# Kernel tuning notes

Hardware: AMD Instinct MI355X
Metric: run time of the kernel (lower is better)

## Reference

```python
import jax, jax.numpy as jnp
import numpy as np

N_NODES = 100000   # number of graph nodes
N_EDGES = 1600000  # adjacency nnz (avg degree 16)
FEAT_NNZ = 1600000 # sparse feature nnz (~16 per node)
F_IN = 512
F_OUT = 128


def setup_inputs() -> dict:
    key = jax.random.key(0)
    k1, k2, k3, k4, k5, k6 = jax.random.split(key, 6)
    adj_indices = jax.random.randint(k1, (2, N_EDGES), 0, N_NODES, dtype=jnp.int64 if jax.config.jax_enable_x64 else jnp.int32)
    adj_values = jax.random.uniform(k2, (N_EDGES,), dtype=jnp.float32)
    feat_rows = jax.random.randint(k3, (FEAT_NNZ,), 0, N_NODES)
    feat_cols = jax.random.randint(k4, (FEAT_NNZ,), 0, F_IN)
    feat_values = jax.random.uniform(k5, (FEAT_NNZ,), dtype=jnp.float32)
    # xavier_uniform init of the dense weight, as in the torch module
    bound = float(np.sqrt(6.0 / (F_IN + F_OUT)))
    weight = jax.random.uniform(k6, (F_IN, F_OUT), dtype=jnp.float32, minval=-bound, maxval=bound)
    return {
        "adj_indices": adj_indices,
        "adj_values": adj_values,
        "feat_rows": feat_rows,
        "feat_cols": feat_cols,
        "feat_values": feat_values,
        "weight": weight,
        "num_nodes": N_NODES,
    }


def _spmm(rows, cols, vals, num_rows, dense):
    """COO sparse [num_rows, ?] @ dense [?, K] -> [num_rows, K]."""
    msgs = vals[:, None] * dense[cols]          # [nnz, K] gather + scale
    return jax.ops.segment_sum(msgs, rows, num_segments=num_rows)


def reference(adj_indices, adj_values, feat_rows, feat_cols, feat_values, weight, num_nodes):
    # spmm(features, W): sparse [N, F_in] @ [F_in, F_out]
    base_features = _spmm(feat_rows, feat_cols, feat_values, num_nodes, weight)
    # spmm(A_hat, base): sparse [N, N] @ [N, F_out]  -- neighbor aggregation
    out = _spmm(adj_indices[0], adj_indices[1], adj_values, num_nodes, base_features)
    return out
```

## Files before the change

kernel.cpp:

```cpp
#include <hip/hip_runtime.h>
#include <stdint.h>

#define N_NODES 100000
#define F_IN    512
#define F_OUT   128
#define BROWS   128
#define NBKT    ((N_NODES + BROWS - 1) / BROWS)
#define CAP     2560
#define EPB     2048

typedef unsigned short     u16;
typedef unsigned int       u32;
typedef unsigned long long u64;
typedef long long          i64;

__device__ __forceinline__ float b2f(u16 u) {
    union { u32 i; float f; } x; x.i = ((u32)u) << 16; return x.f;
}
__device__ __forceinline__ u16 f2b(float f) {
    u32 i = __float_as_uint(f);
    return (u16)((i + 0x7fffu + ((i >> 16) & 1u)) >> 16);
}
__device__ __forceinline__ float blo(u32 u) { return __uint_as_float(u << 16); }
__device__ __forceinline__ float bhi(u32 u) { return __uint_as_float(u & 0xFFFF0000u); }
__device__ __forceinline__ int ld_idx(const void* p, int i, int w64) {
    return w64 ? (int)((const i64*)p)[i] : ((const int*)p)[i];
}
__device__ __forceinline__ u16 ld_val_bf(const void* p, int i, int f32) {
    return f32 ? f2b(((const float*)p)[i]) : ((const u16*)p)[i];
}
__device__ __forceinline__ void ld_idx4(int* r, const void* p, int g, int w64) {
    if (w64) {
        const i64* q = (const i64*)p + 4 * (size_t)g;
        longlong2 a = *(const longlong2*)q;
        longlong2 b = *(const longlong2*)(q + 2);
        r[0] = (int)a.x; r[1] = (int)a.y; r[2] = (int)b.x; r[3] = (int)b.y;
    } else {
        int4 a = *(const int4*)((const int*)p + 4 * (size_t)g);
        r[0] = a.x; r[1] = a.y; r[2] = a.z; r[3] = a.w;
    }
}
__device__ __forceinline__ void ld_val4(u32* v, const void* p, int g, int f32) {
    if (f32) {
        float4 a = *(const float4*)((const float*)p + 4 * (size_t)g);
        v[0] = f2b(a.x); v[1] = f2b(a.y); v[2] = f2b(a.z); v[3] = f2b(a.w);
    } else {
        ushort4 a = *(const ushort4*)((const u16*)p + 4 * (size_t)g);
        v[0] = a.x; v[1] = a.y; v[2] = a.z; v[3] = a.w;
    }
}

__global__ void sniff_k(const u16* __restrict__ w, const u32* __restrict__ adj,
                        const u32* __restrict__ frows, int* __restrict__ flags,
                        int* __restrict__ gcurF, int* __restrict__ gcurA) {
    int t = threadIdx.x;
    if (t < 64) {
        u32 e0 = (w[t]      >> 7) & 0xFF;
        u32 e1 = (w[64 + t] >> 7) & 0xFF;
        u64 bad = __ballot((e0 > 0x7B) || (e1 > 0x7B));
        u64 za = __ballot(adj[2 * t + 1] == 0u);
        u64 zf = __ballot(frows[2 * t + 1] == 0u);
        if (t == 0) {
            flags[0] = (bad != 0);
            flags[1] = (__popcll(za) >= 32);
            flags[2] = (__popcll(zf) >= 32);
        }
    }
    for (int i = t; i < NBKT; i += 256) { gcurF[i] = 0; gcurA[i] = 0; }
}

__global__ __launch_bounds__(512, 6) void binF_k(const void* __restrict__ frows,
        const void* __restrict__ fcols, const void* __restrict__ fvals, int M,
        const int* __restrict__ flags, int* __restrict__ gcurF, u32* __restrict__ fbkt) {
    __shared__ int hist[NBKT];
    __shared__ int hbase[NBKT];
    int t = threadIdx.x;
    for (int i = t; i < NBKT; i += 512) hist[i] = 0;
    __syncthreads();
    int f64 = flags[2], f32 = flags[0];
    int start = blockIdx.x * EPB;
    int end = min(start + EPB, M);
    int g = (start >> 2) + t;
    int e0 = 4 * g;
    int r[4] = {-1, -1, -1, -1};
    int c[4]; u32 v[4];
    if (e0 + 3 < end) {
        ld_idx4(r, frows, g, f64);
        ld_idx4(c, fcols, g, f64);
        ld_val4(v, fvals, g, f32);
    } else {
        #pragma unroll
        for (int j = 0; j < 4; ++j) if (e0 + j < end) {
            r[j] = ld_idx(frows, e0 + j, f64);
            c[j] = ld_idx(fcols, e0 + j, f64);
            v[j] = ld_val_bf(fvals, e0 + j, f32);
        }
    }
    #pragma unroll
    for (int j = 0; j < 4; ++j) if (r[j] >= 0) atomicAdd(&hist[r[j] >> 7], 1);
    __syncthreads();
    for (int i = t; i < NBKT; i += 512) {
        int h = hist[i];
        hbase[i] = h ? atomicAdd(&gcurF[i], h) : 0;
        hist[i] = 0;
    }
    __syncthreads();
    #pragma unroll
    for (int j = 0; j < 4; ++j) if (r[j] >= 0) {
        int b = r[j] >> 7;
        int pos = hbase[b] + atomicAdd(&hist[b], 1);
        if (pos < CAP)
            fbkt[(size_t)b * CAP + pos] = (v[j] << 16) | ((u32)(r[j] & 127) << 9) | (u32)c[j];
    }
}

union S1Mem {
    struct { int hist[NBKT]; int hbase[NBKT]; } bin;
    struct { u32 csr[CAP]; int hcnt[BROWS]; int roff[BROWS + 1]; int cur[BROWS]; } s1;
};

__global__ __launch_bounds__(512, 4) void binA_s1_k(
        const void* __restrict__ adjbase, const void* __restrict__ avals, int E, int nAb,
        const int* __restrict__ flags, int* __restrict__ gcurA, u64* __restrict__ abkt,
        const int* __restrict__ cntF, const u32* __restrict__ fbkt,
        const void* __restrict__ W, u16* __restrict__ base) {
    __shared__ S1Mem sm;
    int t = threadIdx.x;
    int f32 = flags[0];
    if ((int)blockIdx.x < nAb) {
        for (int i = t; i < NBKT; i += 512) sm.bin.hist[i] = 0;
        __syncthreads();
        int a64 = flags[1];
        const void* acols = a64 ? (const void*)((const i64*)adjbase + E)
                                : (const void*)((const int*)adjbase + E);
        int start = blockIdx.x * EPB;
        int end = min(start + EPB, E);
        int g = (start >> 2) + t;
        int e0 = 4 * g;
        int r[4] = {-1, -1, -1, -1};
        int c[4]; u32 v[4];
        if (e0 + 3 < end) {
            ld_idx4(r, adjbase, g, a64);
            ld_idx4(c, acols, g, a64);
            ld_val4(v, avals, g, f32);
        } else {
            #pragma unroll
            for (int j = 0; j < 4; ++j) if (e0 + j < end) {
                r[j] = ld_idx(adjbase, e0 + j, a64);
                c[j] = ld_idx(acols, e0 + j, a64);
                v[j] = ld_val_bf(avals, e0 + j, f32);
            }
        }
        #pragma unroll
        for (int j = 0; j < 4; ++j) if (r[j] >= 0) atomicAdd(&sm.bin.hist[r[j] >> 7], 1);
        __syncthreads();
        for (int i = t; i < NBKT; i += 512) {
            int h = sm.bin.hist[i];
            sm.bin.hbase[i] = h ? atomicAdd(&gcurA[i], h) : 0;
            sm.bin.hist[i] = 0;
        }
        __syncthreads();
        #pragma unroll
        for (int j = 0; j < 4; ++j) if (r[j] >= 0) {
            int b = r[j] >> 7;
            int pos = sm.bin.hbase[b] + atomicAdd(&sm.bin.hist[b], 1);
            if (pos < CAP)
                abkt[(size_t)b * CAP + pos] =
                    ((u64)v[j] << 24) | ((u64)(r[j] & 127) << 17) | (u64)(u32)c[j];
        }
        return;
    }
    int b = blockIdx.x - nAb;
    int n = cntF[b]; if (n > CAP) n = CAP;
    const u32* ed = fbkt + (size_t)b * CAP;
    if (t < BROWS) sm.s1.hcnt[t] = 0;
    __syncthreads();
    u32 pb[5];
    #pragma unroll
    for (int k = 0; k < 5; ++k) { int i = t + k * 512; pb[k] = (i < n) ? ed[i] : 0u; }
    #pragma unroll
    for (int k = 0; k < 5; ++k) { int i = t + k * 512; if (i < n) atomicAdd(&sm.s1.hcnt[(pb[k] >> 9) & 127], 1); }
    __syncthreads();
    if (t < 64) {
        int h0 = sm.s1.hcnt[2 * t], h1 = sm.s1.hcnt[2 * t + 1];
        int s = h0 + h1, v2 = s;
        #pragma unroll
        for (int off = 1; off < 64; off <<= 1) {
            int u = __shfl_up(v2, off);
            if (t >= off) v2 += u;
        }
        int excl = v2 - s;
        sm.s1.roff[2 * t] = excl;     sm.s1.roff[2 * t + 1] = excl + h0;
        sm.s1.cur[2 * t]  = excl;     sm.s1.cur[2 * t + 1]  = excl + h0;
        if (t == 63) sm.s1.roff[128] = v2;
    }
    __syncthreads();
    #pragma unroll
    for (int k = 0; k < 5; ++k) {
        int i = t + k * 512;
        if (i < n) {
            u32 p = pb[k];
            int pos = atomicAdd(&sm.s1.cur[(p >> 9) & 127], 1);
            sm.s1.csr[pos] = p;
        }
    }
    __syncthreads();
    int wave = t >> 6, lane = t & 63, g16 = lane >> 4, l16 = lane & 15;
    #pragma unroll
    for (int set = 0; set < 4; ++set) {
        int row = set * 32 + wave * 4 + g16;
        int s = sm.s1.roff[row], e = sm.s1.roff[row + 1];
        float a[8] = {0.f, 0.f, 0.f, 0.f, 0.f, 0.f, 0.f, 0.f};
        if (f32) {
            const float* Wf = (const float*)W;
            for (int j0 = s; j0 < e; j0 += 4) {
                u32 p[4]; float4 qa[4], qb[4];
                #pragma unroll
                for (int k = 0; k < 4; ++k) { int jk = j0 + k; p[k] = sm.s1.csr[jk < e ? jk : e - 1]; }
                #pragma unroll
                for (int k = 0; k < 4; ++k) {
                    const float* wp = Wf + (size_t)(p[k] & 0x1FF) * F_OUT + l16 * 8;
                    qa[k] = *(const float4*)wp;
                    qb[k] = *(const float4*)(wp + 4);
                }
                #pragma unroll
                for (int k = 0; k < 4; ++k) {
                    float v = (j0 + k < e) ? b2f((u16)(p[k] >> 16)) : 0.f;
                    a[0] += v * qa[k].x; a[1] += v * qa[k].y;
                    a[2] += v * qa[k].z; a[3] += v * qa[k].w;
                    a[4] += v * qb[k].x; a[5] += v * qb[k].y;
                    a[6] += v * qb[k].z; a[7] += v * qb[k].w;
                }
            }
        } else {
            const u16* Wb = (const u16*)W;
            for (int j0 = s; j0 < e; j0 += 8) {
                u32 p[8]; uint4 q[8];
                #pragma unroll
                for (int k = 0; k < 8; ++k) { int jk = j0 + k; p[k] = sm.s1.csr[jk < e ? jk : e - 1]; }
                #pragma unroll
                for (int k = 0; k < 8; ++k)
                    q[k] = *(const uint4*)(Wb + (size_t)(p[k] & 0x1FF) * F_OUT + l16 * 8);
                #pragma unroll
                for (int k = 0; k < 8; ++k) {
                    float v = (j0 + k < e) ? b2f((u16)(p[k] >> 16)) : 0.f;
                    a[0] += v * blo(q[k].x); a[1] += v * bhi(q[k].x);
                    a[2] += v * blo(q[k].y); a[3] += v * bhi(q[k].y);
                    a[4] += v * blo(q[k].z); a[5] += v * bhi(q[k].z);
                    a[6] += v * blo(q[k].w); a[7] += v * bhi(q[k].w);
                }
            }
        }
        int gr = b * BROWS + row;
        if (gr < N_NODES) {
            uint4 o;
            o.x = (u32)f2b(a[0]) | ((u32)f2b(a[1]) << 16);
            o.y = (u32)f2b(a[2]) | ((u32)f2b(a[3]) << 16);
            o.z = (u32)f2b(a[4]) | ((u32)f2b(a[5]) << 16);
            o.w = (u32)f2b(a[6]) | ((u32)f2b(a[7]) << 16);
            *(uint4*)(base + (size_t)gr * F_OUT + l16 * 8) = o;
        }
    }
}

__global__ __launch_bounds__(512, 4) void stage2_k(const int* __restrict__ cnt,
        const u64* __restrict__ bkts, const u16* __restrict__ base,
        const int* __restrict__ flags, void* __restrict__ out) {
    __shared__ u64 csr[CAP];
    __shared__ int hcnt[BROWS];
    __shared__ int roff[BROWS + 1];
    __shared__ int cur[BROWS];
    int t = threadIdx.x;
    int b = blockIdx.x;
    int n = cnt[b]; if (n > CAP) n = CAP;
    const u64* ed = bkts + (size_t)b * CAP;
    if (t < BROWS) hcnt[t] = 0;
    __syncthreads();
    u64 pb[5];
    #pragma unroll
    for (int k = 0; k < 5; ++k) { int i = t + k * 512; pb[k] = (i < n) ? ed[i] : 0ull; }
    #pragma unroll
    for (int k = 0; k < 5; ++k) { int i = t + k * 512; if (i < n) atomicAdd(&hcnt[(int)((pb[k] >> 17) & 127)], 1); }
    __syncthreads();
    if (t < 64) {
        int h0 = hcnt[2 * t], h1 = hcnt[2 * t + 1];
        int s = h0 + h1, v2 = s;
        #pragma unroll
        for (int off = 1; off < 64; off <<= 1) {
            int u = __shfl_up(v2, off);
            if (t >= off) v2 += u;
        }
        int excl = v2 - s;
        roff[2 * t] = excl;     roff[2 * t + 1] = excl + h0;
        cur[2 * t]  = excl;     cur[2 * t + 1]  = excl + h0;
        if (t == 63) roff[128] = v2;
    }
    __syncthreads();
    #pragma unroll
    for (int k = 0; k < 5; ++k) {
        int i = t + k * 512;
        if (i < n) {
            u64 p = pb[k];
            int pos = atomicAdd(&cur[(int)((p >> 17) & 127)], 1);
            csr[pos] = p;
        }
    }
    __syncthreads();
    int wave = t >> 6, lane = t & 63, g16 = lane >> 4, l16 = lane & 15;
    int f32o = flags[0];
    #pragma unroll
    for (int set = 0; set < 4; ++set) {
        int row = set * 32 + wave * 4 + g16;
        int s = roff[row], e = roff[row + 1];
        float a[8] = {0.f, 0.f, 0.f, 0.f, 0.f, 0.f, 0.f, 0.f};
        for (int j0 = s; j0 < e; j0 += 8) {
            u64 p[8]; uint4 q[8];
            #pragma unroll
            for (int k = 0; k < 8; ++k) { int jk = j0 + k; p[k] = csr[jk < e ? jk : e - 1]; }
            #pragma unroll
            for (int k = 0; k < 8; ++k)
                q[k] = *(const uint4*)(base + (size_t)(u32)(p[k] & 0x1FFFF) * F_OUT + l16 * 8);
            #pragma unroll
            for (int k = 0; k < 8; ++k) {
                float v = (j0 + k < e) ? b2f((u16)(p[k] >> 24)) : 0.f;
                a[0] += v * blo(q[k].x); a[1] += v * bhi(q[k].x);
                a[2] += v * blo(q[k].y); a[3] += v * bhi(q[k].y);
                a[4] += v * blo(q[k].z); a[5] += v * bhi(q[k].z);
                a[6] += v * blo(q[k].w); a[7] += v * bhi(q[k].w);
            }
        }
        int gr = b * BROWS + row;
        if (gr < N_NODES) {
            if (f32o) {
                float* op = (float*)out + (size_t)gr * F_OUT + l16 * 8;
                float4 o0, o1;
                o0.x = a[0]; o0.y = a[1]; o0.z = a[2]; o0.w = a[3];
                o1.x = a[4]; o1.y = a[5]; o1.z = a[6]; o1.w = a[7];
                *(float4*)op = o0;
                *(float4*)(op + 4) = o1;
            } else {
                uint4 o;
                o.x = (u32)f2b(a[0]) | ((u32)f2b(a[1]) << 16);
                o.y = (u32)f2b(a[2]) | ((u32)f2b(a[3]) << 16);
                o.z = (u32)f2b(a[4]) | ((u32)f2b(a[5]) << 16);
                o.w = (u32)f2b(a[6]) | ((u32)f2b(a[7]) << 16);
                *(uint4*)((u16*)out + (size_t)gr * F_OUT + l16 * 8) = o;
            }
        }
    }
}

extern "C" void kernel_launch(void* const* d_in, const int* in_sizes, int n_in,
                              void* d_out, int out_size, void* d_ws, size_t ws_size,
                              hipStream_t stream) {
    const void* adj_idx   = d_in[0];
    const void* adj_vals  = d_in[1];
    const void* feat_rows = d_in[2];
    const void* feat_cols = d_in[3];
    const void* feat_vals = d_in[4];
    const void* weight    = d_in[5];

    const int E = in_sizes[0] / 2;
    const int M = in_sizes[2];

    char* ws = (char*)d_ws;
    size_t o = 0;
    auto alloc = [&](size_t b) { size_t r = o; o += (b + 255) & ~(size_t)255; return r; };
    int* gcurF = (int*)(ws + alloc((size_t)NBKT * 4));
    int* gcurA = (int*)(ws + alloc((size_t)NBKT * 4));
    int* flags = (int*)(ws + alloc(4 * 4));
    u32* fbkt  = (u32*)(ws + alloc((size_t)NBKT * CAP * 4));
    u64* abkt  = (u64*)(ws + alloc((size_t)NBKT * CAP * 8));
    u16* base  = (u16*)(ws + alloc((size_t)N_NODES * F_OUT * 2));
    (void)ws_size;

    const int nFb = (M + EPB - 1) / EPB;
    const int nAb = (E + EPB - 1) / EPB;

    sniff_k<<<1, 256, 0, stream>>>((const u16*)weight, (const u32*)adj_idx,
                                   (const u32*)feat_rows, flags, gcurF, gcurA);
    binF_k<<<nFb, 512, 0, stream>>>(feat_rows, feat_cols, feat_vals, M,
                                    flags, gcurF, fbkt);
    binA_s1_k<<<nAb + NBKT, 512, 0, stream>>>(adj_idx, adj_vals, E, nAb,
                                              flags, gcurA, abkt,
                                              gcurF, fbkt, weight, base);
    stage2_k<<<NBKT, 512, 0, stream>>>(gcurA, abkt, base, flags, d_out);
}
```

Before: 262.8 us.

## Gather rows via global_load_lds into LDS staging in both SpMM stages

Both gather loops now use direct global-to-LDS async loads (global_load_lds) into per-wave LDS buffers instead of register gathers, followed by LDS reads for the FMA. A new kernel converts a bf16 weight to fp32 once so stage 1 always gathers fp32 rows. The aim is to cut VGPR pressure and issue overhead on the random row gathers. In exchange it adds 64KB and 32KB of shared memory per block, which lowers occupancy, and each batch of four loads is followed by a full waitcnt(0), which serialises the loads behind the compute.

```diff
diff --git a/kernel.cpp b/kernel.cpp
--- a/kernel.cpp
+++ b/kernel.cpp
@@ -14,6 +14,10 @@
 typedef unsigned long long u64;
 typedef long long          i64;
 
+typedef const __attribute__((address_space(1))) void* gas_t;
+typedef __attribute__((address_space(3))) void*       las_t;
+#define WAIT0() do { __builtin_amdgcn_s_waitcnt(0); __builtin_amdgcn_sched_barrier(0); } while (0)
+
 __device__ __forceinline__ float b2f(u16 u) {
     union { u32 i; float f; } x; x.i = ((u32)u) << 16; return x.f;
 }
@@ -29,6 +33,7 @@
 __device__ __forceinline__ u16 ld_val_bf(const void* p, int i, int f32) {
     return f32 ? f2b(((const float*)p)[i]) : ((const u16*)p)[i];
 }
+
 __device__ __forceinline__ void ld_idx4(int* r, const void* p, int g, int w64) {
     if (w64) {
         const i64* q = (const i64*)p + 4 * (size_t)g;
@@ -67,6 +72,16 @@
         }
     }
     for (int i = t; i < NBKT; i += 256) { gcurF[i] = 0; gcurA[i] = 0; }
+}
+
+__global__ void wconv_k(const int* __restrict__ flags, const u16* __restrict__ wsrc,
+                        float* __restrict__ Wf) {
+    if (flags[0]) return;
+    int i = (blockIdx.x * 256 + threadIdx.x) * 4;
+    ushort4 a = *(const ushort4*)(wsrc + i);
+    float4 o;
+    o.x = b2f(a.x); o.y = b2f(a.y); o.z = b2f(a.z); o.w = b2f(a.w);
+    *(float4*)(Wf + i) = o;
 }
 
 __global__ __launch_bounds__(512, 6) void binF_k(const void* __restrict__ frows,
@@ -123,8 +138,9 @@
         const void* __restrict__ adjbase, const void* __restrict__ avals, int E, int nAb,
         const int* __restrict__ flags, int* __restrict__ gcurA, u64* __restrict__ abkt,
         const int* __restrict__ cntF, const u32* __restrict__ fbkt,
-        const void* __restrict__ W, u16* __restrict__ base) {
+        const void* __restrict__ W, const float* __restrict__ Wf, u16* __restrict__ base) {
     __shared__ S1Mem sm;
+    __shared__ float s1buf[8 * 2048];
     int t = threadIdx.x;
     int f32 = flags[0];
     if ((int)blockIdx.x < nAb) {
@@ -205,59 +221,54 @@
         }
     }
     __syncthreads();
-    int wave = t >> 6, lane = t & 63, g16 = lane >> 4, l16 = lane & 15;
+    int w = t >> 6, lane = t & 63, g16 = lane >> 4, l16 = lane & 15;
+    const float* Wsrc = f32 ? (const float*)W : Wf;
+    float* wbuf = s1buf + (size_t)w * 2048;
+    int hsel = l16 >> 3;
+    int foff = g16 * 64 + (l16 & 7) * 8;
     #pragma unroll
     for (int set = 0; set < 4; ++set) {
-        int row = set * 32 + wave * 4 + g16;
+        int row = set * 32 + w * 4 + g16;
         int s = sm.s1.roff[row], e = sm.s1.roff[row + 1];
-        float a[8] = {0.f, 0.f, 0.f, 0.f, 0.f, 0.f, 0.f, 0.f};
-        if (f32) {
-            const float* Wf = (const float*)W;
-            for (int j0 = s; j0 < e; j0 += 4) {
-                u32 p[4]; float4 qa[4], qb[4];
+        float a0 = 0.f, a1 = 0.f, a2 = 0.f, a3 = 0.f, a4 = 0.f, a5 = 0.f, a6 = 0.f, a7 = 0.f;
+        int trips = (e > s) ? ((e - s + 3) >> 2) : 0;
+        int B = trips;
+        B = max(B, __shfl_xor(B, 16));
+        B = max(B, __shfl_xor(B, 32));
+        int fb = (e > s) ? s : 0;
+        for (int bb = 0; bb < B; ++bb) {
+            WAIT0();
+            u32 pk[4];
+            #pragma unroll
+            for (int k = 0; k < 4; ++k) {
+                int j = s + bb * 4 + k;
+                pk[k] = sm.s1.csr[j < e ? j : fb];
+                const float* ga = Wsrc + (size_t)(pk[k] & 0x1FF) * F_OUT + l16 * 4;
                 #pragma unroll
-                for (int k = 0; k < 4; ++k) { int jk = j0 + k; p[k] = sm.s1.csr[jk < e ? jk : e - 1]; }
-                #pragma unroll
-                for (int k = 0; k < 4; ++k) {
-                    const float* wp = Wf + (size_t)(p[k] & 0x1FF) * F_OUT + l16 * 8;
-                    qa[k] = *(const float4*)wp;
-                    qb[k] = *(const float4*)(wp + 4);
-                }
-                #pragma unroll
-                for (int k = 0; k < 4; ++k) {
-                    float v = (j0 + k < e) ? b2f((u16)(p[k] >> 16)) : 0.f;
-                    a[0] += v * qa[k].x; a[1] += v * qa[k].y;
-                    a[2] += v * qa[k].z; a[3] += v * qa[k].w;
-                    a[4] += v * qb[k].x; a[5] += v * qb[k].y;
-                    a[6] += v * qb[k].z; a[7] += v * qb[k].w;
-                }
-            }
-        } else {
-            const u16* Wb = (const u16*)W;
-            for (int j0 = s; j0 < e; j0 += 8) {
-                u32 p[8]; uint4 q[8];
-                #pragma unroll
-                for (int k = 0; k < 8; ++k) { int jk = j0 + k; p[k] = sm.s1.csr[jk < e ? jk : e - 1]; }
-                #pragma unroll
-                for (int k = 0; k < 8; ++k)
-                    q[k] = *(const uint4*)(Wb + (size_t)(p[k] & 0x1FF) * F_OUT + l16 * 8);
-                #pragma unroll
-                for (int k = 0; k < 8; ++k) {
-                    float v = (j0 + k < e) ? b2f((u16)(p[k] >> 16)) : 0.f;
-                    a[0] += v * blo(q[k].x); a[1] += v * bhi(q[k].x);
-                    a[2] += v * blo(q[k].y); a[3] += v * bhi(q[k].y);
-                    a[4] += v * blo(q[k].z); a[5] += v * bhi(q[k].z);
-                    a[6] += v * blo(q[k].w); a[7] += v * bhi(q[k].w);
-                }
+                for (int h = 0; h < 2; ++h)
+                    __builtin_amdgcn_global_load_lds(
+                        (gas_t)(ga + h * 64),
+                        (las_t)(wbuf + (k * 2 + h) * 256), 16, 0, 0);
+            }
+            WAIT0();
+            #pragma unroll
+            for (int k = 0; k < 4; ++k) {
+                int j = s + bb * 4 + k;
+                float v = (j < e) ? b2f((u16)(pk[k] >> 16)) : 0.f;
+                const float* lp = wbuf + (k * 2 + hsel) * 256 + foff;
+                float4 q1 = *(const float4*)lp;
+                float4 q2 = *(const float4*)(lp + 4);
+                a0 += v * q1.x; a1 += v * q1.y; a2 += v * q1.z; a3 += v * q1.w;
+                a4 += v * q2.x; a5 += v * q2.y; a6 += v * q2.z; a7 += v * q2.w;
             }
         }
         int gr = b * BROWS + row;
         if (gr < N_NODES) {
             uint4 o;
-            o.x = (u32)f2b(a[0]) | ((u32)f2b(a[1]) << 16);
-            o.y = (u32)f2b(a[2]) | ((u32)f2b(a[3]) << 16);
-            o.z = (u32)f2b(a[4]) | ((u32)f2b(a[5]) << 16);
-            o.w = (u32)f2b(a[6]) | ((u32)f2b(a[7]) << 16);
+            o.x = (u32)f2b(a0) | ((u32)f2b(a1) << 16);
+            o.y = (u32)f2b(a2) | ((u32)f2b(a3) << 16);
+            o.z = (u32)f2b(a4) | ((u32)f2b(a5) << 16);
+            o.w = (u32)f2b(a6) | ((u32)f2b(a7) << 16);
             *(uint4*)(base + (size_t)gr * F_OUT + l16 * 8) = o;
         }
     }
@@ -270,6 +281,7 @@
     __shared__ int hcnt[BROWS];
     __shared__ int roff[BROWS + 1];
     __shared__ int cur[BROWS];
+    __shared__ u16 s2buf[8 * 2048];
     int t = threadIdx.x;
     int b = blockIdx.x;
     int n = cnt[b]; if (n > CAP) n = CAP;
@@ -306,27 +318,40 @@
         }
     }
     __syncthreads();
-    int wave = t >> 6, lane = t & 63, g16 = lane >> 4, l16 = lane & 15;
+    int w = t >> 6, lane = t & 63, g16 = lane >> 4, l16 = lane & 15;
     int f32o = flags[0];
+    u16* wbuf = s2buf + (size_t)w * 2048;
+    int uoff = g16 * 128 + l16 * 8;
     #pragma unroll
     for (int set = 0; set < 4; ++set) {
-        int row = set * 32 + wave * 4 + g16;
+        int row = set * 32 + w * 4 + g16;
         int s = roff[row], e = roff[row + 1];
-        float a[8] = {0.f, 0.f, 0.f, 0.f, 0.f, 0.f, 0.f, 0.f};
-        for (int j0 = s; j0 < e; j0 += 8) {
-            u64 p[8]; uint4 q[8];
+        float a0 = 0.f, a1 = 0.f, a2 = 0.f, a3 = 0.f, a4 = 0.f, a5 = 0.f, a6 = 0.f, a7 = 0.f;
+        int trips = (e > s) ? ((e - s + 3) >> 2) : 0;
+        int B = trips;
+        B = max(B, __shfl_xor(B, 16));
+        B = max(B, __shfl_xor(B, 32));
+        int fb = (e > s) ? s : 0;
+        for (int bb = 0; bb < B; ++bb) {
+            WAIT0();
+            u64 pk[4];
             #pragma unroll
-            for (int k = 0; k < 8; ++k) { int jk = j0 + k; p[k] = csr[jk < e ? jk : e - 1]; }
+            for (int k = 0; k < 4; ++k) {
+                int j = s + bb * 4 + k;
+                pk[k] = csr[j < e ? j : fb];
+                const u16* ga = base + (size_t)(u32)(pk[k] & 0x1FFFF) * F_OUT + l16 * 8;
+                __builtin_amdgcn_global_load_lds((gas_t)ga, (las_t)(wbuf + k * 512), 16, 0, 0);
+            }
+            WAIT0();
             #pragma unroll
-            for (int k = 0; k < 8; ++k)
-                q[k] = *(const uint4*)(base + (size_t)(u32)(p[k] & 0x1FFFF) * F_OUT + l16 * 8);
-            #pragma unroll
-            for (int k = 0; k < 8; ++k) {
-                float v = (j0 + k < e) ? b2f((u16)(p[k] >> 24)) : 0.f;
-                a[0] += v * blo(q[k].x); a[1] += v * bhi(q[k].x);
-                a[2] += v * blo(q[k].y); a[3] += v * bhi(q[k].y);
-                a[4] += v * blo(q[k].z); a[5] += v * bhi(q[k].z);
-                a[6] += v * blo(q[k].w); a[7] += v * bhi(q[k].w);
+            for (int k = 0; k < 4; ++k) {
+                int j = s + bb * 4 + k;
+                float v = (j < e) ? b2f((u16)(pk[k] >> 24)) : 0.f;
+                uint4 q = *(const uint4*)(wbuf + k * 512 + uoff);
+                a0 += v * blo(q.x); a1 += v * bhi(q.x);
+                a2 += v * blo(q.y); a3 += v * bhi(q.y);
+                a4 += v * blo(q.z); a5 += v * bhi(q.z);
+                a6 += v * blo(q.w); a7 += v * bhi(q.w);
             }
         }
         int gr = b * BROWS + row;
@@ -334,16 +359,16 @@
             if (f32o) {
                 float* op = (float*)out + (size_t)gr * F_OUT + l16 * 8;
                 float4 o0, o1;
-                o0.x = a[0]; o0.y = a[1]; o0.z = a[2]; o0.w = a[3];
-                o1.x = a[4]; o1.y = a[5]; o1.z = a[6]; o1.w = a[7];
+                o0.x = a0; o0.y = a1; o0.z = a2; o0.w = a3;
+                o1.x = a4; o1.y = a5; o1.z = a6; o1.w = a7;
                 *(float4*)op = o0;
                 *(float4*)(op + 4) = o1;
             } else {
                 uint4 o;
-                o.x = (u32)f2b(a[0]) | ((u32)f2b(a[1]) << 16);
-                o.y = (u32)f2b(a[2]) | ((u32)f2b(a[3]) << 16);
-                o.z = (u32)f2b(a[4]) | ((u32)f2b(a[5]) << 16);
-                o.w = (u32)f2b(a[6]) | ((u32)f2b(a[7]) << 16);
+                o.x = (u32)f2b(a0) | ((u32)f2b(a1) << 16);
+                o.y = (u32)f2b(a2) | ((u32)f2b(a3) << 16);
+                o.z = (u32)f2b(a4) | ((u32)f2b(a5) << 16);
+                o.w = (u32)f2b(a6) | ((u32)f2b(a7) << 16);
                 *(uint4*)((u16*)out + (size_t)gr * F_OUT + l16 * 8) = o;
             }
         }
@@ -369,6 +394,7 @@
     int* gcurF = (int*)(ws + alloc((size_t)NBKT * 4));
     int* gcurA = (int*)(ws + alloc((size_t)NBKT * 4));
     int* flags = (int*)(ws + alloc(4 * 4));
+    float* Wf  = (float*)(ws + alloc((size_t)F_IN * F_OUT * 4));
     u32* fbkt  = (u32*)(ws + alloc((size_t)NBKT * CAP * 4));
     u64* abkt  = (u64*)(ws + alloc((size_t)NBKT * CAP * 8));
     u16* base  = (u16*)(ws + alloc((size_t)N_NODES * F_OUT * 2));
@@ -379,10 +405,11 @@
 
     sniff_k<<<1, 256, 0, stream>>>((const u16*)weight, (const u32*)adj_idx,
                                    (const u32*)feat_rows, flags, gcurF, gcurA);
+    wconv_k<<<64, 256, 0, stream>>>(flags, (const u16*)weight, Wf);
     binF_k<<<nFb, 512, 0, stream>>>(feat_rows, feat_cols, feat_vals, M,
                                     flags, gcurF, fbkt);
     binA_s1_k<<<nAb + NBKT, 512, 0, stream>>>(adj_idx, adj_vals, E, nAb,
                                               flags, gcurA, abkt,
-                                              gcurF, fbkt, weight, base);
+                                              gcurF, fbkt, weight, Wf, base);
     stage2_k<<<NBKT, 512, 0, stream>>>(gcurA, abkt, base, flags, d_out);
 }
```

Result: no change. 265.9 us (+1.2%).

## Stage weight matrix in LDS with persistent stage1 and merge binning kernels

Applied to the files above, without the earlier changes.

Feature and adjacency binning now run in one kernel, and the feature SpMM moves into a separate persistent kernel with 256 blocks. Each block copies the whole bf16 weight matrix into padded shared memory once and then serves its bucket rows' gathers from LDS instead of global/L2. The change trades the earlier overlap of adjacency binning with stage1 for LDS-resident weights. It also cuts the bf16 inner unroll from 8 to 4 and uses about 140KB of LDS per block, which limits occupancy to one block per CU.

```diff
diff --git a/kernel.cpp b/kernel.cpp
--- a/kernel.cpp
+++ b/kernel.cpp
@@ -8,6 +8,7 @@
 #define NBKT    ((N_NODES + BROWS - 1) / BROWS)
 #define CAP     2560
 #define EPB     2048
+#define WPAD    136
 
 typedef unsigned short     u16;
 typedef unsigned int       u32;
@@ -29,6 +30,7 @@
 __device__ __forceinline__ u16 ld_val_bf(const void* p, int i, int f32) {
     return f32 ? f2b(((const float*)p)[i]) : ((const u16*)p)[i];
 }
+
 __device__ __forceinline__ void ld_idx4(int* r, const void* p, int g, int w64) {
     if (w64) {
         const i64* q = (const i64*)p + 4 * (size_t)g;
@@ -69,71 +71,59 @@
     for (int i = t; i < NBKT; i += 256) { gcurF[i] = 0; gcurA[i] = 0; }
 }
 
-__global__ __launch_bounds__(512, 6) void binF_k(const void* __restrict__ frows,
-        const void* __restrict__ fcols, const void* __restrict__ fvals, int M,
-        const int* __restrict__ flags, int* __restrict__ gcurF, u32* __restrict__ fbkt) {
+__global__ __launch_bounds__(512, 4) void binFA_k(
+        const void* __restrict__ frows, const void* __restrict__ fcols,
+        const void* __restrict__ fvals, int M, int nFb,
+        const void* __restrict__ adjbase, const void* __restrict__ avals, int E,
+        const int* __restrict__ flags, int* __restrict__ gcurF, int* __restrict__ gcurA,
+        u32* __restrict__ fbkt, u64* __restrict__ abkt) {
     __shared__ int hist[NBKT];
     __shared__ int hbase[NBKT];
     int t = threadIdx.x;
     for (int i = t; i < NBKT; i += 512) hist[i] = 0;
     __syncthreads();
-    int f64 = flags[2], f32 = flags[0];
-    int start = blockIdx.x * EPB;
-    int end = min(start + EPB, M);
-    int g = (start >> 2) + t;
-    int e0 = 4 * g;
-    int r[4] = {-1, -1, -1, -1};
-    int c[4]; u32 v[4];
-    if (e0 + 3 < end) {
-        ld_idx4(r, frows, g, f64);
-        ld_idx4(c, fcols, g, f64);
-        ld_val4(v, fvals, g, f32);
+    int f32 = flags[0];
+    if ((int)blockIdx.x < nFb) {
+        int f64 = flags[2];
+        int start = blockIdx.x * EPB;
+        int end = min(start + EPB, M);
+        int g = (start >> 2) + t;
+        int e0 = 4 * g;
+        int r[4] = {-1, -1, -1, -1};
+        int c[4]; u32 v[4];
+        if (e0 + 3 < end) {
+            ld_idx4(r, frows, g, f64);
+            ld_idx4(c, fcols, g, f64);
+            ld_val4(v, fvals, g, f32);
+        } else {
+            #pragma unroll
+            for (int j = 0; j < 4; ++j) if (e0 + j < end) {
+                r[j] = ld_idx(frows, e0 + j, f64);
+                c[j] = ld_idx(fcols, e0 + j, f64);
+                v[j] = ld_val_bf(fvals, e0 + j, f32);
+            }
+        }
+        #pragma unroll
+        for (int j = 0; j < 4; ++j) if (r[j] >= 0) atomicAdd(&hist[r[j] >> 7], 1);
+        __syncthreads();
+        for (int i = t; i < NBKT; i += 512) {
+            int h = hist[i];
+            hbase[i] = h ? atomicAdd(&gcurF[i], h) : 0;
+            hist[i] = 0;
+        }
+        __syncthreads();
+        #pragma unroll
+        for (int j = 0; j < 4; ++j) if (r[j] >= 0) {
+            int b = r[j] >> 7;
+            int pos = hbase[b] + atomicAdd(&hist[b], 1);
+            if (pos < CAP)
+                fbkt[(size_t)b * CAP + pos] = (v[j] << 16) | ((u32)(r[j] & 127) << 9) | (u32)c[j];
+        }
     } else {
-        #pragma unroll
-        for (int j = 0; j < 4; ++j) if (e0 + j < end) {
-            r[j] = ld_idx(frows, e0 + j, f64);
-            c[j] = ld_idx(fcols, e0 + j, f64);
-            v[j] = ld_val_bf(fvals, e0 + j, f32);
-        }
-    }
-    #pragma unroll
-    for (int j = 0; j < 4; ++j) if (r[j] >= 0) atomicAdd(&hist[r[j] >> 7], 1);
-    __syncthreads();
-    for (int i = t; i < NBKT; i += 512) {
-        int h = hist[i];
-        hbase[i] = h ? atomicAdd(&gcurF[i], h) : 0;
-        hist[i] = 0;
-    }
-    __syncthreads();
-    #pragma unroll
-    for (int j = 0; j < 4; ++j) if (r[j] >= 0) {
-        int b = r[j] >> 7;
-        int pos = hbase[b] + atomicAdd(&hist[b], 1);
-        if (pos < CAP)
-            fbkt[(size_t)b * CAP + pos] = (v[j] << 16) | ((u32)(r[j] & 127) << 9) | (u32)c[j];
-    }
-}
-
-union S1Mem {
-    struct { int hist[NBKT]; int hbase[NBKT]; } bin;
-    struct { u32 csr[CAP]; int hcnt[BROWS]; int roff[BROWS + 1]; int cur[BROWS]; } s1;
-};
-
-__global__ __launch_bounds__(512, 4) void binA_s1_k(
-        const void* __restrict__ adjbase, const void* __restrict__ avals, int E, int nAb,
-        const int* __restrict__ flags, int* __restrict__ gcurA, u64* __restrict__ abkt,
-        const int* __restrict__ cntF, const u32* __restrict__ fbkt,
-        const void* __restrict__ W, u16* __restrict__ base) {
-    __shared__ S1Mem sm;
-    int t = threadIdx.x;
-    int f32 = flags[0];
-    if ((int)blockIdx.x < nAb) {
-        for (int i = t; i < NBKT; i += 512) sm.bin.hist[i] = 0;
-        __syncthreads();
         int a64 = flags[1];
         const void* acols = a64 ? (const void*)((const i64*)adjbase + E)
                                 : (const void*)((const int*)adjbase + E);
-        int start = blockIdx.x * EPB;
+        int start = ((int)blockIdx.x - nFb) * EPB;
         int end = min(start + EPB, E);
         int g = (start >> 2) + t;
         int e0 = 4 * g;
@@ -152,114 +142,134 @@
             }
         }
         #pragma unroll
-        for (int j = 0; j < 4; ++j) if (r[j] >= 0) atomicAdd(&sm.bin.hist[r[j] >> 7], 1);
+        for (int j = 0; j < 4; ++j) if (r[j] >= 0) atomicAdd(&hist[r[j] >> 7], 1);
         __syncthreads();
         for (int i = t; i < NBKT; i += 512) {
-            int h = sm.bin.hist[i];
-            sm.bin.hbase[i] = h ? atomicAdd(&gcurA[i], h) : 0;
-            sm.bin.hist[i] = 0;
+            int h = hist[i];
+            hbase[i] = h ? atomicAdd(&gcurA[i], h) : 0;
+            hist[i] = 0;
         }
         __syncthreads();
         #pragma unroll
         for (int j = 0; j < 4; ++j) if (r[j] >= 0) {
             int b = r[j] >> 7;
-            int pos = sm.bin.hbase[b] + atomicAdd(&sm.bin.hist[b], 1);
+            int pos = hbase[b] + atomicAdd(&hist[b], 1);
             if (pos < CAP)
                 abkt[(size_t)b * CAP + pos] =
                     ((u64)v[j] << 24) | ((u64)(r[j] & 127) << 17) | (u64)(u32)c[j];
         }
-        return;
-    }
-    int b = blockIdx.x - nAb;
-    int n = cntF[b]; if (n > CAP) n = CAP;
-    const u32* ed = fbkt + (size_t)b * CAP;
-    if (t < BROWS) sm.s1.hcnt[t] = 0;
-    __syncthreads();
-    u32 pb[5];
-    #pragma unroll
-    for (int k = 0; k < 5; ++k) { int i = t + k * 512; pb[k] = (i < n) ? ed[i] : 0u; }
-    #pragma unroll
-    for (int k = 0; k < 5; ++k) { int i = t + k * 512; if (i < n) atomicAdd(&sm.s1.hcnt[(pb[k] >> 9) & 127], 1); }
-    __syncthreads();
-    if (t < 64) {
-        int h0 = sm.s1.hcnt[2 * t], h1 = sm.s1.hcnt[2 * t + 1];
-        int s = h0 + h1, v2 = s;
-        #pragma unroll
-        for (int off = 1; off < 64; off <<= 1) {
-            int u = __shfl_up(v2, off);
-            if (t >= off) v2 += u;
-        }
-        int excl = v2 - s;
-        sm.s1.roff[2 * t] = excl;     sm.s1.roff[2 * t + 1] = excl + h0;
-        sm.s1.cur[2 * t]  = excl;     sm.s1.cur[2 * t + 1]  = excl + h0;
-        if (t == 63) sm.s1.roff[128] = v2;
-    }
-    __syncthreads();
-    #pragma unroll
-    for (int k = 0; k < 5; ++k) {
-        int i = t + k * 512;
-        if (i < n) {
-            u32 p = pb[k];
-            int pos = atomicAdd(&sm.s1.cur[(p >> 9) & 127], 1);
-            sm.s1.csr[pos] = p;
-        }
-    }
-    __syncthreads();
-    int wave = t >> 6, lane = t & 63, g16 = lane >> 4, l16 = lane & 15;
-    #pragma unroll
-    for (int set = 0; set < 4; ++set) {
-        int row = set * 32 + wave * 4 + g16;
-        int s = sm.s1.roff[row], e = sm.s1.roff[row + 1];
-        float a[8] = {0.f, 0.f, 0.f, 0.f, 0.f, 0.f, 0.f, 0.f};
-        if (f32) {
-            const float* Wf = (const float*)W;
-            for (int j0 = s; j0 < e; j0 += 4) {
-                u32 p[4]; float4 qa[4], qb[4];
-                #pragma unroll
-                for (int k = 0; k < 4; ++k) { int jk = j0 + k; p[k] = sm.s1.csr[jk < e ? jk : e - 1]; }
-                #pragma unroll
-                for (int k = 0; k < 4; ++k) {
-                    const float* wp = Wf + (size_t)(p[k] & 0x1FF) * F_OUT + l16 * 8;
-                    qa[k] = *(const float4*)wp;
-                    qb[k] = *(const float4*)(wp + 4);
+    }
+}
+
+__global__ __launch_bounds__(512, 1) void stage1_k(const int* __restrict__ cnt,
+        const u32* __restrict__ bkts, const void* __restrict__ W,
+        const int* __restrict__ flags, u16* __restrict__ base) {
+    __shared__ u16 Wlds[F_IN * WPAD];
+    __shared__ u32 csr[CAP];
+    __shared__ int hcnt[BROWS];
+    __shared__ int roff[BROWS + 1];
+    __shared__ int cur[BROWS];
+    int t = threadIdx.x;
+    int f32 = flags[0];
+    if (!f32) {
+        const u16* Wb = (const u16*)W;
+        for (int idx = t; idx < F_IN * 16; idx += 512) {
+            int r = idx >> 4, c = idx & 15;
+            uint4 q = *(const uint4*)(Wb + r * F_OUT + c * 8);
+            *(uint4*)&Wlds[r * WPAD + c * 8] = q;
+        }
+    }
+    int w = t >> 6, lane = t & 63, g16 = lane >> 4, l16 = lane & 15;
+    for (int b = blockIdx.x; b < NBKT; b += gridDim.x) {
+        int n = cnt[b]; if (n > CAP) n = CAP;
+        const u32* ed = bkts + (size_t)b * CAP;
+        if (t < BROWS) hcnt[t] = 0;
+        __syncthreads();
+        u32 pb[5];
+        #pragma unroll
+        for (int k = 0; k < 5; ++k) { int i = t + k * 512; pb[k] = (i < n) ? ed[i] : 0u; }
+        #pragma unroll
+        for (int k = 0; k < 5; ++k) { int i = t + k * 512; if (i < n) atomicAdd(&hcnt[(pb[k] >> 9) & 127], 1); }
+        __syncthreads();
+        if (t < 64) {
+            int h0 = hcnt[2 * t], h1 = hcnt[2 * t + 1];
+            int s = h0 + h1, v2 = s;
+            #pragma unroll
+            for (int off = 1; off < 64; off <<= 1) {
+                int u = __shfl_up(v2, off);
+                if (t >= off) v2 += u;
+            }
+            int excl = v2 - s;
+            roff[2 * t] = excl;     roff[2 * t + 1] = excl + h0;
+            cur[2 * t]  = excl;     cur[2 * t + 1]  = excl + h0;
+            if (t == 63) roff[128] = v2;
+        }
+        __syncthreads();
+        #pragma unroll
+        for (int k = 0; k < 5; ++k) {
+            int i = t + k * 512;
+            if (i < n) {
+                u32 p = pb[k];
+                int pos = atomicAdd(&cur[(p >> 9) & 127], 1);
+                csr[pos] = p;
+            }
+        }
+        __syncthreads();
+        #pragma unroll
+        for (int set = 0; set < 4; ++set) {
+            int row = set * 32 + w * 4 + g16;
+            int s = roff[row], e = roff[row + 1];
+            float a0 = 0.f, a1 = 0.f, a2 = 0.f, a3 = 0.f, a4 = 0.f, a5 = 0.f, a6 = 0.f, a7 = 0.f;
+            if (f32) {
+                const float* Wf = (const float*)W;
+                for (int j0 = s; j0 < e; j0 += 4) {
+                    u32 p[4]; float4 qa[4], qb[4];
+                    #pragma unroll
+                    for (int k = 0; k < 4; ++k) { int jk = j0 + k; p[k] = csr[jk < e ? jk : e - 1]; }
+                    #pragma unroll
+                    for (int k = 0; k < 4; ++k) {
+                        const float* wp = Wf + (size_t)(p[k] & 0x1FF) * F_OUT + l16 * 8;
+                        qa[k] = *(const float4*)wp;
+                        qb[k] = *(const float4*)(wp + 4);
+                    }
+                    #pragma unroll
+                    for (int k = 0; k < 4; ++k) {
+                        float v = (j0 + k < e) ? b2f((u16)(p[k] >> 16)) : 0.f;
+                        a0 += v * qa[k].x; a1 += v * qa[k].y;
+                        a2 += v * qa[k].z; a3 += v * qa[k].w;
+                        a4 += v * qb[k].x; a5 += v * qb[k].y;
+                        a6 += v * qb[k].z; a7 += v * qb[k].w;
+                    }
                 }
-                #pragma unroll
-                for (int k = 0; k < 4; ++k) {
-                    float v = (j0 + k < e) ? b2f((u16)(p[k] >> 16)) : 0.f;
-                    a[0] += v * qa[k].x; a[1] += v * qa[k].y;
-                    a[2] += v * qa[k].z; a[3] += v * qa[k].w;
-                    a[4] += v * qb[k].x; a[5] += v * qb[k].y;
-                    a[6] += v * qb[k].z; a[7] += v * qb[k].w;
+            } else {
+                for (int j0 = s; j0 < e; j0 += 4) {
+                    u32 p[4]; uint4 q[4];
+                    #pragma unroll
+                    for (int k = 0; k < 4; ++k) { int jk = j0 + k; p[k] = csr[jk < e ? jk : e - 1]; }
+                    #pragma unroll
+                    for (int k = 0; k < 4; ++k)
+                        q[k] = *(const uint4*)&Wlds[(p[k] & 0x1FF) * WPAD + l16 * 8];
+                    #pragma unroll
+                    for (int k = 0; k < 4; ++k) {
+                        float v = (j0 + k < e) ? b2f((u16)(p[k] >> 16)) : 0.f;
+                        a0 += v * blo(q[k].x); a1 += v * bhi(q[k].x);
+                        a2 += v * blo(q[k].y); a3 += v * bhi(q[k].y);
+                        a4 += v * blo(q[k].z); a5 += v * bhi(q[k].z);
+                        a6 += v * blo(q[k].w); a7 += v * bhi(q[k].w);
+                    }
                 }
             }
-        } else {
-            const u16* Wb = (const u16*)W;
-            for (int j0 = s; j0 < e; j0 += 8) {
-                u32 p[8]; uint4 q[8];
-                #pragma unroll
-                for (int k = 0; k < 8; ++k) { int jk = j0 + k; p[k] = sm.s1.csr[jk < e ? jk : e - 1]; }
-                #pragma unroll
-                for (int k = 0; k < 8; ++k)
-                    q[k] = *(const uint4*)(Wb + (size_t)(p[k] & 0x1FF) * F_OUT + l16 * 8);
-                #pragma unroll
-                for (int k = 0; k < 8; ++k) {
-                    float v = (j0 + k < e) ? b2f((u16)(p[k] >> 16)) : 0.f;
-                    a[0] += v * blo(q[k].x); a[1] += v * bhi(q[k].x);
-                    a[2] += v * blo(q[k].y); a[3] += v * bhi(q[k].y);
-                    a[4] += v * blo(q[k].z); a[5] += v * bhi(q[k].z);
-                    a[6] += v * blo(q[k].w); a[7] += v * bhi(q[k].w);
-                }
-            }
-        }
-        int gr = b * BROWS + row;
-        if (gr < N_NODES) {
-            uint4 o;
-            o.x = (u32)f2b(a[0]) | ((u32)f2b(a[1]) << 16);
-            o.y = (u32)f2b(a[2]) | ((u32)f2b(a[3]) << 16);
-            o.z = (u32)f2b(a[4]) | ((u32)f2b(a[5]) << 16);
-            o.w = (u32)f2b(a[6]) | ((u32)f2b(a[7]) << 16);
-            *(uint4*)(base + (size_t)gr * F_OUT + l16 * 8) = o;
-        }
+            int gr = b * BROWS + row;
+            if (gr < N_NODES) {
+                uint4 o;
+                o.x = (u32)f2b(a0) | ((u32)f2b(a1) << 16);
+                o.y = (u32)f2b(a2) | ((u32)f2b(a3) << 16);
+                o.z = (u32)f2b(a4) | ((u32)f2b(a5) << 16);
+                o.w = (u32)f2b(a6) | ((u32)f2b(a7) << 16);
+                *(uint4*)(base + (size_t)gr * F_OUT + l16 * 8) = o;
+            }
+        }
+        __syncthreads();
     }
 }
 
@@ -312,7 +322,7 @@
     for (int set = 0; set < 4; ++set) {
         int row = set * 32 + wave * 4 + g16;
         int s = roff[row], e = roff[row + 1];
-        float a[8] = {0.f, 0.f, 0.f, 0.f, 0.f, 0.f, 0.f, 0.f};
+        float a0 = 0.f, a1 = 0.f, a2 = 0.f, a3 = 0.f, a4 = 0.f, a5 = 0.f, a6 = 0.f, a7 = 0.f;
         for (int j0 = s; j0 < e; j0 += 8) {
             u64 p[8]; uint4 q[8];
             #pragma unroll
@@ -323,10 +333,10 @@
             #pragma unroll
             for (int k = 0; k < 8; ++k) {
                 float v = (j0 + k < e) ? b2f((u16)(p[k] >> 24)) : 0.f;
-                a[0] += v * blo(q[k].x); a[1] += v * bhi(q[k].x);
-                a[2] += v * blo(q[k].y); a[3] += v * bhi(q[k].y);
-                a[4] += v * blo(q[k].z); a[5] += v * bhi(q[k].z);
-                a[6] += v * blo(q[k].w); a[7] += v * bhi(q[k].w);
+                a0 += v * blo(q[k].x); a1 += v * bhi(q[k].x);
+                a2 += v * blo(q[k].y); a3 += v * bhi(q[k].y);
+                a4 += v * blo(q[k].z); a5 += v * bhi(q[k].z);
+                a6 += v * blo(q[k].w); a7 += v * bhi(q[k].w);
             }
         }
         int gr = b * BROWS + row;
@@ -334,16 +344,16 @@
             if (f32o) {
                 float* op = (float*)out + (size_t)gr * F_OUT + l16 * 8;
                 float4 o0, o1;
-                o0.x = a[0]; o0.y = a[1]; o0.z = a[2]; o0.w = a[3];
-                o1.x = a[4]; o1.y = a[5]; o1.z = a[6]; o1.w = a[7];
+                o0.x = a0; o0.y = a1; o0.z = a2; o0.w = a3;
+                o1.x = a4; o1.y = a5; o1.z = a6; o1.w = a7;
                 *(float4*)op = o0;
                 *(float4*)(op + 4) = o1;
             } else {
                 uint4 o;
-                o.x = (u32)f2b(a[0]) | ((u32)f2b(a[1]) << 16);
-                o.y = (u32)f2b(a[2]) | ((u32)f2b(a[3]) << 16);
-                o.z = (u32)f2b(a[4]) | ((u32)f2b(a[5]) << 16);
-                o.w = (u32)f2b(a[6]) | ((u32)f2b(a[7]) << 16);
+                o.x = (u32)f2b(a0) | ((u32)f2b(a1) << 16);
+                o.y = (u32)f2b(a2) | ((u32)f2b(a3) << 16);
+                o.z = (u32)f2b(a4) | ((u32)f2b(a5) << 16);
+                o.w = (u32)f2b(a6) | ((u32)f2b(a7) << 16);
                 *(uint4*)((u16*)out + (size_t)gr * F_OUT + l16 * 8) = o;
             }
         }
@@ -379,10 +389,9 @@
 
     sniff_k<<<1, 256, 0, stream>>>((const u16*)weight, (const u32*)adj_idx,
                                    (const u32*)feat_rows, flags, gcurF, gcurA);
-    binF_k<<<nFb, 512, 0, stream>>>(feat_rows, feat_cols, feat_vals, M,
-                                    flags, gcurF, fbkt);
-    binA_s1_k<<<nAb + NBKT, 512, 0, stream>>>(adj_idx, adj_vals, E, nAb,
-                                              flags, gcurA, abkt,
-                                              gcurF, fbkt, weight, base);
+    binFA_k<<<nFb + nAb, 512, 0, stream>>>(feat_rows, feat_cols, feat_vals, M, nFb,
+                                           adj_idx, adj_vals, E,
+                                           flags, gcurF, gcurA, fbkt, abkt);
+    stage1_k<<<256, 512, 0, stream>>>(gcurF, fbkt, weight, flags, base);
     stage2_k<<<NBKT, 512, 0, stream>>>(gcurA, abkt, base, flags, d_out);
 }
```

After: 254.0 us. 3.4% less time.
